# Kernel tuning notes

Measured on AMD Instinct MI355X. Metric: run time of the kernel, lower is better.

The kernel has to match this reference:

```python
import jax, jax.numpy as jnp
import numpy as np

B, M, T, G = 32, 12, 512, 256
PPH = 60  # points_per_hour -> sigma init 2/PPH


def setup_inputs() -> dict:
    key = jax.random.key(0)
    k1, k2, k3 = jax.random.split(key, 3)
    y = jax.random.normal(k1, (B, M, T), dtype=jnp.float32)
    x = jax.random.uniform(k2, (B, T), dtype=jnp.float32)  # observation times in [0,1)
    mask = jax.random.randint(k3, (B, M, T), 0, 2).astype(jnp.bool_)
    grid = jnp.linspace(0.0, 1.0, G, dtype=jnp.float32)  # fixed evaluation grid
    sigma = 2.0 * (1.0 / PPH) * jnp.ones(2, dtype=jnp.float32)  # trainable RBF scales
    return {"y": y, "x": x, "mask": mask, "grid": grid, "sigma": sigma}


def reference(y, x, mask, grid, sigma):
    # y, mask: [B,M,T]; x: [B,T]; grid: [G]; sigma: [2]
    Bs, Ms, Ts = y.shape
    Gs = grid.shape[0]
    # squared distance grid vs points: [B,G,T]
    dist = (grid[None, :, None] - x[:, None, :]) ** 2
    # RBF weights per channel (density, value): [B,G,T,2]; independent of modality
    wt = jnp.exp(-0.5 * dist[..., None] / (sigma ** 2))
    # stack density mask and values: [B,M,T,2]
    y_out = jnp.stack([mask.astype(y.dtype), y], axis=-1)
    # weighted sum over observed points (avoids materializing [B,M,G,T,2]): [B,M,G,2]
    func = jnp.einsum('bmtc,bgtc->bmgc', y_out, wt)
    density = func[..., :1]
    conv = func[..., 1:]
    out = jnp.concatenate([density, conv / (density + 1e-8)], axis=-1)  # [B,M,G,2]
    out = jnp.transpose(out, (0, 1, 3, 2)).reshape(Bs, 2 * Ms, Gs)  # [B,2M,G]
    return jnp.transpose(out, (0, 2, 1))  # [B,G,2M]
```

## Files before the change

### kernel.cpp

```cpp
#include <hip/hip_runtime.h>

#define B_ 32
#define M_ 12
#define T_ 512
#define G_ 256

#define GS 16
#define NBLK 512
#define TPAIR 256
#define ROWW 18


using h2 = decltype(__builtin_amdgcn_cvt_pkrtz(0.f, 0.f));

__device__ __forceinline__ float fdot2f(h2 a, h2 b, float c) {
#if __has_builtin(__builtin_amdgcn_fdot2)
    return __builtin_amdgcn_fdot2(a, b, c, false);
#else
    return c + (float)a[0] * (float)b[0] + (float)a[1] * (float)b[1];
#endif
}

template <int D, int N, int IMM>
__device__ __forceinline__ void red_step(float2* U, int ls) {
    const bool bit = (ls & D) != 0;
#pragma unroll
    for (int i = 0; i < N / 2; ++i) {
        const float2 lo = U[i], hi = U[i + N / 2];
        const float2 snd = bit ? lo : hi;
        float2 rcv;
        rcv.x = __uint_as_float(
            (unsigned)__builtin_amdgcn_ds_swizzle((int)__float_as_uint(snd.x), IMM));
        rcv.y = __uint_as_float(
            (unsigned)__builtin_amdgcn_ds_swizzle((int)__float_as_uint(snd.y), IMM));
        const float2 kp = bit ? hi : lo;
        U[i] = make_float2(kp.x + rcv.x, kp.y + rcv.y);
    }
}

template <int N>
__device__ __forceinline__ void red_step32(float2* U, int ls) {
    const bool bit = (ls & 32) != 0;
#pragma unroll
    for (int i = 0; i < N / 2; ++i) {
        const float2 lo = U[i], hi = U[i + N / 2];
        const float2 snd = bit ? lo : hi;
        float2 rcv;
#if __has_builtin(__builtin_amdgcn_permlane32_swap)
        {
            auto rx = __builtin_amdgcn_permlane32_swap(
                __float_as_uint(snd.x), __float_as_uint(snd.x), false, false);
            auto ry = __builtin_amdgcn_permlane32_swap(
                __float_as_uint(snd.y), __float_as_uint(snd.y), false, false);
            rcv.x = __uint_as_float(bit ? rx[0] : rx[1]);
            rcv.y = __uint_as_float(bit ? ry[0] : ry[1]);
        }
#else
        rcv.x = __shfl_xor(snd.x, 32, 64);
        rcv.y = __shfl_xor(snd.y, 32, 64);
#endif
        const float2 kp = bit ? hi : lo;
        U[i] = make_float2(kp.x + rcv.x, kp.y + rcv.y);
    }
}

__global__ __launch_bounds__(512, 4) void k_fused(
    const float* __restrict__ y, const float* __restrict__ x,
    const int* __restrict__ mask, const float* __restrict__ grid,
    const float* __restrict__ sigma, float* __restrict__ out)
{
    __shared__ unsigned int sy[TPAIR * ROWW];
    __shared__ unsigned int sm[TPAIR * ROWW];

    const int bid = blockIdx.x;
    const int w   = ((bid & 7) << 6) | (bid >> 3);
    const int b   = w >> 4;
    const int gb  = (w & 15) * GS;

    const int tid = threadIdx.x;
    const int gq  = tid >> 6;
    const int ls  = tid & 63;

    float2 xp[4];
#pragma unroll
    for (int k = 0; k < 4; ++k)
        xp[k] = *(const float2*)&x[b * T_ + 2 * (ls + 64 * k)];

#pragma unroll
    for (int it = 0; it < 6; ++it) {
        const int i  = tid + 512 * it;
        const int m  = i >> 8;
        const int tp = i & 255;
        const float2 yv = *(const float2*)&y[(b * M_ + m) * T_ + 2 * tp];
        auto yh = __builtin_amdgcn_cvt_pkrtz(yv.x, yv.y);
        sy[tp * ROWW + m] = __builtin_bit_cast(unsigned int, yh);
        const int2 mv = *(const int2*)&mask[(b * M_ + m) * T_ + 2 * tp];
        sm[tp * ROWW + m] = (mv.x ? 0x3C00u : 0u) | (mv.y ? 0x3C000000u : 0u);
    }
    __syncthreads();

    float gv[2];
#pragma unroll
    for (int h = 0; h < 2; ++h) gv[h] = grid[gb + gq + 8 * h];
    const float s0 = sigma[0], s1 = sigma[1];
    const float LOG2E = 1.4426950408889634f;
    const float c0 = (-0.5f / (s0 * s0)) * LOG2E;
    const float c1 = (-0.5f / (s1 * s1)) * LOG2E;

    float accD[2][12], accC[2][12];
#pragma unroll
    for (int h = 0; h < 2; ++h)
#pragma unroll
        for (int m = 0; m < 12; ++m) { accD[h][m] = 0.f; accC[h][m] = 0.f; }

#pragma unroll
    for (int k = 0; k < 4; ++k) {
        const int tp = ls + 64 * k;
        const float2 xv = xp[k];
        h2 w0[2], w1[2];
#pragma unroll
        for (int h = 0; h < 2; ++h) {
            const float d0 = gv[h] - xv.x, d1 = gv[h] - xv.y;
            const float p0 = d0 * d0, p1 = d1 * d1;
            w0[h] = __builtin_amdgcn_cvt_pkrtz(__builtin_amdgcn_exp2f(p0 * c0),
                                               __builtin_amdgcn_exp2f(p1 * c0));
            w1[h] = __builtin_amdgcn_cvt_pkrtz(__builtin_amdgcn_exp2f(p0 * c1),
                                               __builtin_amdgcn_exp2f(p1 * c1));
        }
        const unsigned int* ry = &sy[tp * ROWW];
        const unsigned int* rm = &sm[tp * ROWW];
#pragma unroll
        for (int j = 0; j < 6; ++j) {
            const uint2 yv2 = *(const uint2*)&ry[2 * j];
            const uint2 mv2 = *(const uint2*)&rm[2 * j];
            const h2 yp0 = __builtin_bit_cast(h2, yv2.x);
            const h2 yp1 = __builtin_bit_cast(h2, yv2.y);
            const h2 mp0 = __builtin_bit_cast(h2, mv2.x);
            const h2 mp1 = __builtin_bit_cast(h2, mv2.y);
#pragma unroll
            for (int h = 0; h < 2; ++h) {
                accD[h][2 * j]     = fdot2f(mp0, w0[h], accD[h][2 * j]);
                accC[h][2 * j]     = fdot2f(yp0, w1[h], accC[h][2 * j]);
                accD[h][2 * j + 1] = fdot2f(mp1, w0[h], accD[h][2 * j + 1]);
                accC[h][2 * j + 1] = fdot2f(yp1, w1[h], accC[h][2 * j + 1]);
            }
        }
    }

    float2 U[32];
#pragma unroll
    for (int mm = 0; mm < 16; ++mm)
#pragma unroll
        for (int h = 0; h < 2; ++h)
            U[mm * 2 + h] = (mm < 12) ? make_float2(accD[h][mm], accC[h][mm])
                                      : make_float2(0.f, 0.f);

    red_step32<32>(U, ls);
    red_step<16, 16, 0x401F>(U, ls);
    red_step<8,   8, 0x201F>(U, ls);
    red_step<4,   4, 0x101F>(U, ls);
    red_step<2,   2, 0x081F>(U, ls);
    {
        float2 rcv;
        rcv.x = __uint_as_float(
            (unsigned)__builtin_amdgcn_ds_swizzle((int)__float_as_uint(U[0].x), 0x041F));
        rcv.y = __uint_as_float(
            (unsigned)__builtin_amdgcn_ds_swizzle((int)__float_as_uint(U[0].y), 0x041F));
        U[0].x += rcv.x;
        U[0].y += rcv.y;
    }

    const int mm = ls >> 2;
    const int h  = (ls >> 1) & 1;
    if ((ls & 1) == 0 && mm < 12) {
        const int g = gb + gq + 8 * h;
        const float dens = U[0].x;
        float2 o;
        o.x = dens;
        o.y = U[0].y / (dens + 1e-8f);
        *(float2*)&out[(size_t)(b * G_ + g) * (2 * M_) + 2 * mm] = o;
    }
}

extern "C" void kernel_launch(void* const* d_in, const int* in_sizes, int n_in,
                              void* d_out, int out_size, void* d_ws, size_t ws_size,
                              hipStream_t stream) {
    const float* y     = (const float*)d_in[0];
    const float* x     = (const float*)d_in[1];
    const int*   mask  = (const int*)d_in[2];
    const float* grid  = (const float*)d_in[3];
    const float* sigma = (const float*)d_in[4];
    float* out = (float*)d_out;
    (void)d_ws; (void)ws_size;

    k_fused<<<NBLK, 512, 0, stream>>>(y, x, mask, grid, sigma, out);
}
```

Baseline: 13.45 us.

## Skip duplicate exp when sigmas match, shorten cross-lane reduction via LDS

The value-channel RBF weights now reuse the density weights when the two sigma coefficients are equal at runtime. A general fallback still computes them when the sigmas differ. The butterfly reduction is cut to three swizzle stages over only the 12 real modalities, with the last 8-lane sum done through a shared-memory scratch buffer. This needs an extra barrier and about 12KB more LDS. Staging now handles two modalities per thread and writes 64-bit stores to shared memory, which halves the loop iterations.

```diff
diff --git a/kernel.cpp b/kernel.cpp
--- a/kernel.cpp
+++ b/kernel.cpp
@@ -21,47 +21,16 @@
 #endif
 }
 
-template <int D, int N, int IMM>
-__device__ __forceinline__ void red_step(float2* U, int ls) {
-    const bool bit = (ls & D) != 0;
-#pragma unroll
-    for (int i = 0; i < N / 2; ++i) {
-        const float2 lo = U[i], hi = U[i + N / 2];
-        const float2 snd = bit ? lo : hi;
-        float2 rcv;
-        rcv.x = __uint_as_float(
-            (unsigned)__builtin_amdgcn_ds_swizzle((int)__float_as_uint(snd.x), IMM));
-        rcv.y = __uint_as_float(
-            (unsigned)__builtin_amdgcn_ds_swizzle((int)__float_as_uint(snd.y), IMM));
-        const float2 kp = bit ? hi : lo;
-        U[i] = make_float2(kp.x + rcv.x, kp.y + rcv.y);
-    }
-}
-
-template <int N>
-__device__ __forceinline__ void red_step32(float2* U, int ls) {
-    const bool bit = (ls & 32) != 0;
-#pragma unroll
-    for (int i = 0; i < N / 2; ++i) {
-        const float2 lo = U[i], hi = U[i + N / 2];
-        const float2 snd = bit ? lo : hi;
-        float2 rcv;
-#if __has_builtin(__builtin_amdgcn_permlane32_swap)
-        {
-            auto rx = __builtin_amdgcn_permlane32_swap(
-                __float_as_uint(snd.x), __float_as_uint(snd.x), false, false);
-            auto ry = __builtin_amdgcn_permlane32_swap(
-                __float_as_uint(snd.y), __float_as_uint(snd.y), false, false);
-            rcv.x = __uint_as_float(bit ? rx[0] : rx[1]);
-            rcv.y = __uint_as_float(bit ? ry[0] : ry[1]);
-        }
-#else
-        rcv.x = __shfl_xor(snd.x, 32, 64);
-        rcv.y = __shfl_xor(snd.y, 32, 64);
-#endif
-        const float2 kp = bit ? hi : lo;
-        U[i] = make_float2(kp.x + rcv.x, kp.y + rcv.y);
-    }
+__device__ __forceinline__ float2 swz_f2(float2 v, int imm_encoded_as_template);
+
+template <int IMM>
+__device__ __forceinline__ float2 swz2(float2 v) {
+    float2 r;
+    r.x = __uint_as_float(
+        (unsigned)__builtin_amdgcn_ds_swizzle((int)__float_as_uint(v.x), IMM));
+    r.y = __uint_as_float(
+        (unsigned)__builtin_amdgcn_ds_swizzle((int)__float_as_uint(v.y), IMM));
+    return r;
 }
 
 __global__ __launch_bounds__(512, 4) void k_fused(
@@ -71,6 +40,7 @@
 {
     __shared__ unsigned int sy[TPAIR * ROWW];
     __shared__ unsigned int sm[TPAIR * ROWW];
+    __shared__ float dmp[8 * 64 * 3 * 2];
 
     const int bid = blockIdx.x;
     const int w   = ((bid & 7) << 6) | (bid >> 3);
@@ -87,15 +57,23 @@
         xp[k] = *(const float2*)&x[b * T_ + 2 * (ls + 64 * k)];
 
 #pragma unroll
-    for (int it = 0; it < 6; ++it) {
+    for (int it = 0; it < 3; ++it) {
         const int i  = tid + 512 * it;
-        const int m  = i >> 8;
+        const int mp = i >> 8;
         const int tp = i & 255;
-        const float2 yv = *(const float2*)&y[(b * M_ + m) * T_ + 2 * tp];
-        auto yh = __builtin_amdgcn_cvt_pkrtz(yv.x, yv.y);
-        sy[tp * ROWW + m] = __builtin_bit_cast(unsigned int, yh);
-        const int2 mv = *(const int2*)&mask[(b * M_ + m) * T_ + 2 * tp];
-        sm[tp * ROWW + m] = (mv.x ? 0x3C00u : 0u) | (mv.y ? 0x3C000000u : 0u);
+        const int m0 = 2 * mp;
+        const float2 y0 = *(const float2*)&y[(b * M_ + m0) * T_ + 2 * tp];
+        const float2 y1 = *(const float2*)&y[(b * M_ + m0 + 1) * T_ + 2 * tp];
+        uint2 yw;
+        yw.x = __builtin_bit_cast(unsigned int, __builtin_amdgcn_cvt_pkrtz(y0.x, y0.y));
+        yw.y = __builtin_bit_cast(unsigned int, __builtin_amdgcn_cvt_pkrtz(y1.x, y1.y));
+        *(uint2*)&sy[tp * ROWW + 2 * mp] = yw;
+        const int2 ma = *(const int2*)&mask[(b * M_ + m0) * T_ + 2 * tp];
+        const int2 mb = *(const int2*)&mask[(b * M_ + m0 + 1) * T_ + 2 * tp];
+        uint2 mw;
+        mw.x = (ma.x ? 0x3C00u : 0u) | (ma.y ? 0x3C000000u : 0u);
+        mw.y = (mb.x ? 0x3C00u : 0u) | (mb.y ? 0x3C000000u : 0u);
+        *(uint2*)&sm[tp * ROWW + 2 * mp] = mw;
     }
     __syncthreads();
 
@@ -106,6 +84,7 @@
     const float LOG2E = 1.4426950408889634f;
     const float c0 = (-0.5f / (s0 * s0)) * LOG2E;
     const float c1 = (-0.5f / (s1 * s1)) * LOG2E;
+    const bool same = (c0 == c1);
 
     float accD[2][12], accC[2][12];
 #pragma unroll
@@ -124,8 +103,9 @@
             const float p0 = d0 * d0, p1 = d1 * d1;
             w0[h] = __builtin_amdgcn_cvt_pkrtz(__builtin_amdgcn_exp2f(p0 * c0),
                                                __builtin_amdgcn_exp2f(p1 * c0));
-            w1[h] = __builtin_amdgcn_cvt_pkrtz(__builtin_amdgcn_exp2f(p0 * c1),
-                                               __builtin_amdgcn_exp2f(p1 * c1));
+            w1[h] = same ? w0[h]
+                         : __builtin_amdgcn_cvt_pkrtz(__builtin_amdgcn_exp2f(p0 * c1),
+                                                      __builtin_amdgcn_exp2f(p1 * c1));
         }
         const unsigned int* ry = &sy[tp * ROWW];
         const unsigned int* rm = &sm[tp * ROWW];
@@ -147,37 +127,82 @@
         }
     }
 
-    float2 U[32];
-#pragma unroll
-    for (int mm = 0; mm < 16; ++mm)
-#pragma unroll
-        for (int h = 0; h < 2; ++h)
-            U[mm * 2 + h] = (mm < 12) ? make_float2(accD[h][mm], accC[h][mm])
-                                      : make_float2(0.f, 0.f);
-
-    red_step32<32>(U, ls);
-    red_step<16, 16, 0x401F>(U, ls);
-    red_step<8,   8, 0x201F>(U, ls);
-    red_step<4,   4, 0x101F>(U, ls);
-    red_step<2,   2, 0x081F>(U, ls);
-    {
-        float2 rcv;
-        rcv.x = __uint_as_float(
-            (unsigned)__builtin_amdgcn_ds_swizzle((int)__float_as_uint(U[0].x), 0x041F));
-        rcv.y = __uint_as_float(
-            (unsigned)__builtin_amdgcn_ds_swizzle((int)__float_as_uint(U[0].y), 0x041F));
-        U[0].x += rcv.x;
-        U[0].y += rcv.y;
-    }
-
-    const int mm = ls >> 2;
-    const int h  = (ls >> 1) & 1;
-    if ((ls & 1) == 0 && mm < 12) {
-        const int g = gb + gq + 8 * h;
-        const float dens = U[0].x;
+    float2 V[12];
+    {
+        const bool bit = (ls & 32) != 0;
+#pragma unroll
+        for (int mm = 0; mm < 12; ++mm) {
+            const float2 lo = make_float2(accD[0][mm], accC[0][mm]);
+            const float2 hi = make_float2(accD[1][mm], accC[1][mm]);
+            const float2 snd = bit ? lo : hi;
+            float2 rcv;
+#if __has_builtin(__builtin_amdgcn_permlane32_swap)
+            {
+                auto rx = __builtin_amdgcn_permlane32_swap(
+                    __float_as_uint(snd.x), __float_as_uint(snd.x), false, false);
+                auto ry2 = __builtin_amdgcn_permlane32_swap(
+                    __float_as_uint(snd.y), __float_as_uint(snd.y), false, false);
+                rcv.x = __uint_as_float(bit ? rx[0] : rx[1]);
+                rcv.y = __uint_as_float(bit ? ry2[0] : ry2[1]);
+            }
+#else
+            rcv.x = __shfl_xor(snd.x, 32, 64);
+            rcv.y = __shfl_xor(snd.y, 32, 64);
+#endif
+            const float2 kp = bit ? hi : lo;
+            V[mm] = make_float2(kp.x + rcv.x, kp.y + rcv.y);
+        }
+    }
+    float2 W6[6];
+    {
+        const bool bit = (ls & 16) != 0;
+#pragma unroll
+        for (int i = 0; i < 6; ++i) {
+            const float2 lo = V[i], hi = V[i + 6];
+            const float2 snd = bit ? lo : hi;
+            const float2 rcv = swz2<0x401F>(snd);
+            const float2 kp  = bit ? hi : lo;
+            W6[i] = make_float2(kp.x + rcv.x, kp.y + rcv.y);
+        }
+    }
+    float2 Z[3];
+    {
+        const bool bit = (ls & 8) != 0;
+#pragma unroll
+        for (int i = 0; i < 3; ++i) {
+            const float2 lo = W6[i], hi = W6[i + 3];
+            const float2 snd = bit ? lo : hi;
+            const float2 rcv = swz2<0x201F>(snd);
+            const float2 kp  = bit ? hi : lo;
+            Z[i] = make_float2(kp.x + rcv.x, kp.y + rcv.y);
+        }
+    }
+
+    {
+        float* dp = &dmp[(gq * 64 + ls) * 6];
+#pragma unroll
+        for (int s = 0; s < 3; ++s) *(float2*)&dp[2 * s] = Z[s];
+    }
+    __syncthreads();
+
+    if (tid < 8 * 24) {
+        const int wv = tid / 24;
+        const int r  = tid % 24;
+        const int h  = r / 12;
+        const int mm = r % 12;
+        const int base_ls = h * 32 + (mm / 6) * 16 + ((mm % 6) / 3) * 8;
+        const int s = mm % 3;
+        float dens = 0.f, conv = 0.f;
+#pragma unroll
+        for (int k = 0; k < 8; ++k) {
+            const float2 v = *(const float2*)&dmp[((wv * 64 + base_ls + k) * 3 + s) * 2];
+            dens += v.x;
+            conv += v.y;
+        }
+        const int g = gb + wv + 8 * h;
         float2 o;
         o.x = dens;
-        o.y = U[0].y / (dens + 1e-8f);
+        o.y = conv / (dens + 1e-8f);
         *(float2*)&out[(size_t)(b * G_ + g) * (2 * M_) + 2 * mm] = o;
     }
 }
```

Result: faster. 12.60 us (-6.3%).
